# Kernel optimization log

Hardware: AMD Instinct MI355X
Metric: run time of the kernel (lower is better)

Reference implementation:

```python
import jax, jax.numpy as jnp
import numpy as np

N_HEAD = 8
T_THRESHOLD = 0.001


def setup_inputs() -> dict:
    key = jax.random.key(0)
    ks = jax.random.split(key, 5)
    B, N, NL, R = 4, 1024, 4, 256
    C = NL * R
    x = jax.random.normal(ks[0], (B, N, NL, R), dtype=jnp.float32)
    Wc = jax.random.normal(ks[1], (R, 3 * R), dtype=jnp.float32) * (1.0 / np.sqrt(R))
    bc = jnp.zeros((3 * R,), dtype=jnp.float32)
    Wp = jax.random.normal(ks[2], (C, C), dtype=jnp.float32) * (1.0 / np.sqrt(C))
    bp = jnp.zeros((C,), dtype=jnp.float32)
    return {"x": x, "Wc": Wc, "bc": bc, "Wp": Wp, "bp": bp}


def reference(x, Wc, bc, Wp, bp):
    B, N, NL, R = x.shape
    H = N_HEAD
    D = R // H  # head dim
    # shared per-level qkv projection: (B, N, NL, 3R)
    qkv = x @ Wc + bc
    q, k, v = jnp.split(qkv, 3, axis=-1)
    # split heads: (B, N, NL, H, D)
    q = q.reshape(B, N, NL, H, D)
    k = k.reshape(B, N, NL, H, D)
    v = v.reshape(B, N, NL, H, D)
    scale = 1.0 / np.sqrt(D).astype(np.float32)
    # per-level attention scores: (B, NL, H, N, N)
    att = jnp.einsum('bnlhd,bmlhd->blhnm', q, k) * scale
    att = jax.nn.softmax(att, axis=-1)
    # custom post-softmax thresholding (ReLU(softmax - T)); dropout is identity at eval
    att = jax.nn.relu(att - T_THRESHOLD)
    # multiply attentions across levels: low parent attention dooms the child
    comb = jnp.prod(att, axis=1)  # (B, H, N, N)
    # apply combined attention to each level's values: (B, N, NL, H, D)
    y = jnp.einsum('bhnm,bmlhd->bnlhd', comb, v)
    y = y.reshape(B, N, NL * H * D)  # (B, N, C)
    y = y @ Wp + bp  # c_proj; resid dropout identity at eval
    return y.reshape(B, N, NL, R)
```

## Files before the change

kernel.cpp:

```cpp
#include <hip/hip_runtime.h>

#define TTHR 0.001f
#define QSC2 0.25503486f
#define CAP 16
#define YSCALE 8388608.0f
#define YINV   1.1920928955078125e-07f

#if __has_builtin(__builtin_amdgcn_exp2f)
#define EXP2(x) __builtin_amdgcn_exp2f(x)
#else
#define EXP2(x) __expf((x) * 0.6931471805599453f)
#endif

typedef _Float16 half4v __attribute__((ext_vector_type(4)));
typedef _Float16 half8v __attribute__((ext_vector_type(8)));
typedef float f32x4 __attribute__((ext_vector_type(4)));

__device__ __forceinline__ int xcd_bid() {
  return (blockIdx.x & 7) * ((int)gridDim.x >> 3) + ((int)blockIdx.x >> 3);
}

__device__ __forceinline__ void stage_tile_s(const _Float16* __restrict__ gsrc,
                                             int rowstride, _Float16* lds, int tid)
{
  const int lane = tid & 63;
  const int w4 = (tid >> 6) << 2;
#pragma unroll
  for (int r = 0; r < 4; ++r) {
    const int p = (w4 + r) * 64 + lane;
    const int row = p >> 3, xg = p & 7;
    __builtin_amdgcn_global_load_lds(
        (const __attribute__((address_space(1))) void*)(gsrc + row * rowstride + ((xg ^ (row & 7)) << 3)),
        (__attribute__((address_space(3))) void*)(lds + (w4 + r) * 512),
        16, 0, 0);
  }
}

__device__ __forceinline__ void stage_tile64(const _Float16* __restrict__ gsrc,
                                             int rowstride, _Float16* lds, int tid)
{
  const int lane = tid & 63;
  const int w2 = (tid >> 6) << 1;
#pragma unroll
  for (int r = 0; r < 2; ++r) {
    const int p = (w2 + r) * 64 + lane;
    const int row = p >> 3, xg = p & 7;
    __builtin_amdgcn_global_load_lds(
        (const __attribute__((address_space(1))) void*)(gsrc + row * rowstride + ((xg ^ (row & 7)) << 3)),
        (__attribute__((address_space(3))) void*)(lds + (w2 + r) * 512),
        16, 0, 0);
  }
}

__device__ __forceinline__ void stage_q64_512(const _Float16* __restrict__ gsrc,
                                              _Float16* lds, int tid)
{
  const int lane = tid & 63, w = tid >> 6;
  const int p = (w << 6) + lane;
  const int row = p >> 3, xg = p & 7;
  __builtin_amdgcn_global_load_lds(
      (const __attribute__((address_space(1))) void*)(gsrc + row * 64 + ((xg ^ (row & 7)) << 3)),
      (__attribute__((address_space(3))) void*)(lds + (w << 9)),
      16, 0, 0);
}

__device__ __forceinline__ void stage_k128_512(const _Float16* __restrict__ gsrc,
                                               _Float16* lds, int tid)
{
  const int lane = tid & 63, w = tid >> 6;
#pragma unroll
  for (int r = 0; r < 2; ++r) {
    const int p = ((w << 1) + r) * 64 + lane;
    const int row = p >> 3, xg = p & 7;
    __builtin_amdgcn_global_load_lds(
        (const __attribute__((address_space(1))) void*)(gsrc + row * 64 + ((xg ^ (row & 7)) << 3)),
        (__attribute__((address_space(3))) void*)(lds + ((w << 1) + r) * 512),
        16, 0, 0);
  }
}

__global__ __launch_bounds__(256) void k_split_rm(
    const float* __restrict__ in, _Float16* __restrict__ oh,
    _Float16* __restrict__ ol, int n4)
{
  const int i = blockIdx.x * 256 + threadIdx.x;
  if (i >= n4) return;
  float4 v = ((const float4*)in)[i];
  half4v h = {(_Float16)v.x, (_Float16)v.y, (_Float16)v.z, (_Float16)v.w};
  half4v l = {(_Float16)(v.x - (float)h[0]), (_Float16)(v.y - (float)h[1]),
              (_Float16)(v.z - (float)h[2]), (_Float16)(v.w - (float)h[3])};
  ((half4v*)oh)[i] = h;
  ((half4v*)ol)[i] = l;
}

__global__ __launch_bounds__(256) void k_split_tr(
    const float* __restrict__ in, _Float16* __restrict__ oh,
    _Float16* __restrict__ ol, int K, int N)
{
  __shared__ float t[32][33];
  const int nb = N >> 5;
  const int n0 = (blockIdx.x % nb) << 5, k0 = (blockIdx.x / nb) << 5;
  const int r = threadIdx.x >> 3, c4 = (threadIdx.x & 7) << 2;
  float4 v = *(const float4*)&in[(k0 + r) * N + n0 + c4];
  t[r][c4] = v.x; t[r][c4 + 1] = v.y; t[r][c4 + 2] = v.z; t[r][c4 + 3] = v.w;
  __syncthreads();
  float a0 = t[c4][r], a1 = t[c4 + 1][r], a2 = t[c4 + 2][r], a3 = t[c4 + 3][r];
  half4v h = {(_Float16)a0, (_Float16)a1, (_Float16)a2, (_Float16)a3};
  half4v l = {(_Float16)(a0 - (float)h[0]), (_Float16)(a1 - (float)h[1]),
              (_Float16)(a2 - (float)h[2]), (_Float16)(a3 - (float)h[3])};
  *(half4v*)&oh[(n0 + r) * K + k0 + c4] = h;
  *(half4v*)&ol[(n0 + r) * K + k0 + c4] = l;
}

template<int EPI>
__global__ __launch_bounds__(256) void k_gemm_split(
    const _Float16* __restrict__ Ah, const _Float16* __restrict__ Al,
    const _Float16* __restrict__ Bh, const _Float16* __restrict__ Bl,
    const float* __restrict__ bias, int K, int kclog, int nbn,
    float* __restrict__ out, _Float16* __restrict__ Qs,
    _Float16* __restrict__ Ks, float* __restrict__ Vp)
{
  __shared__ __align__(16) _Float16 Asm[3][8192];
  __shared__ __align__(16) _Float16 Bsm[3][4096];
  const int tid = threadIdx.x, lane = tid & 63, w = tid >> 6;
  const int wr = w >> 1, wc = w & 1;
  const int lrow = lane & 15, lk = lane >> 4;
  const int bid = xcd_bid();
  const int mt = bid / nbn, ct = bid % nbn;
  const int m0 = mt << 7, c0 = ct << 6;

  const int nch = 3 << kclog;
  const int kcm = (1 << kclog) - 1;

  auto abase = [&](int c2) -> const _Float16* {
    const int phase = c2 >> kclog, kc = c2 & kcm;
    const _Float16* A = (phase == 2) ? Al : Ah;
    return A + (size_t)m0 * K + (kc << 6);
  };
  auto bbase = [&](int c2) -> const _Float16* {
    const int phase = c2 >> kclog, kc = c2 & kcm;
    const _Float16* B = (phase == 1) ? Bl : Bh;
    return B + (size_t)c0 * K + (kc << 6);
  };

  stage_tile_s(abase(0), K, Asm[0], tid);
  stage_tile64(bbase(0), K, Bsm[0], tid);
  stage_tile_s(abase(1), K, Asm[1], tid);
  stage_tile64(bbase(1), K, Bsm[1], tid);

  f32x4 acc[4][2] = {};
  int cur = 0;
#pragma unroll 1
  for (int ch = 0; ch < nch; ++ch) {
    if (ch + 1 < nch) { asm volatile("s_waitcnt vmcnt(6)" ::: "memory"); }
    else              { asm volatile("s_waitcnt vmcnt(0)" ::: "memory"); }
    __builtin_amdgcn_s_barrier();
    __builtin_amdgcn_sched_barrier(0);
#pragma unroll
    for (int ks = 0; ks < 2; ++ks) {
      half8v af[4], bf[2];
#pragma unroll
      for (int mi = 0; mi < 4; ++mi) {
        const int row = (wr << 6) + (mi << 4) + lrow;
        const int xg = ((ks << 2) + lk) ^ (row & 7);
        af[mi] = *(const half8v*)&Asm[cur][((row << 3) + xg) << 3];
      }
#pragma unroll
      for (int ni = 0; ni < 2; ++ni) {
        const int col = (wc << 5) + (ni << 4) + lrow;
        const int xg = ((ks << 2) + lk) ^ (col & 7);
        bf[ni] = *(const half8v*)&Bsm[cur][((col << 3) + xg) << 3];
      }
#pragma unroll
      for (int mi = 0; mi < 4; ++mi)
#pragma unroll
        for (int ni = 0; ni < 2; ++ni)
          acc[mi][ni] = __builtin_amdgcn_mfma_f32_16x16x32_f16(af[mi], bf[ni], acc[mi][ni], 0, 0, 0);
    }
    if (ch + 2 < nch) {
      int nb = cur + 2; if (nb >= 3) nb -= 3;
      stage_tile_s(abase(ch + 2), K, Asm[nb], tid);
      stage_tile64(bbase(ch + 2), K, Bsm[nb], tid);
    }
    ++cur; if (cur == 3) cur = 0;
  }

#pragma unroll
  for (int ni = 0; ni < 2; ++ni) {
    const int c = c0 + (wc << 5) + (ni << 4) + lrow;
    const float bv = bias[c];
    if (EPI == 0) {
#pragma unroll
      for (int mi = 0; mi < 4; ++mi)
#pragma unroll
        for (int reg = 0; reg < 4; ++reg) {
          const int m = m0 + (wr << 6) + (mi << 4) + (lk << 2) + reg;
          out[m * 1024 + c] = acc[mi][ni][reg] * YINV + bv;
        }
    } else {
      const int part = c >> 8, cc = c & 255;
      const int h = cc >> 5, d = cc & 31;
#pragma unroll
      for (int mi = 0; mi < 4; ++mi)
#pragma unroll
        for (int reg = 0; reg < 4; ++reg) {
          const int m = m0 + (wr << 6) + (mi << 4) + (lk << 2) + reg;
          const int b = m >> 12, n = (m >> 2) & 1023, l = m & 3;
          const int panel = b * 32 + l * 8 + h;
          float v = acc[mi][ni][reg] + bv;
          if (part == 2) {
            Vp[(panel << 15) + n * 32 + d] = v;
          } else {
            _Float16* dst = part ? Ks : Qs;
            if (!part) v *= QSC2;
            _Float16 hv = (_Float16)v;
            _Float16 lv = (_Float16)(v - (float)hv);
            dst[(panel << 16) + n * 64 + d] = hv;
            dst[(panel << 16) + n * 64 + 32 + d] = lv;
          }
        }
    }
  }
}

__global__ __launch_bounds__(512) void k_att(
    const _Float16* __restrict__ Qs, const _Float16* __restrict__ Ks,
    int* __restrict__ ccnt, unsigned short* __restrict__ cidx,
    float* __restrict__ cval)
{
  __shared__ __align__(16) _Float16 Qres[4][4096];
  __shared__ __align__(16) _Float16 Kb[2][8192];
  __shared__ float Zsh[4][64];
  __shared__ float tzs[4][64];
  __shared__ float rz[64];
  __shared__ int lcnt[64];
  const int tid = threadIdx.x, lane = tid & 63, w = tid >> 6;
  const int wr = w >> 2, wc = w & 3;
  const int lrow = lane & 15, lk = lane >> 4;
  const int s = (blockIdx.x & 7) * 64 + ((int)blockIdx.x >> 3);
  const int bh = s >> 4, rt = s & 15;
  const int b = bh >> 3, h = bh & 7;
  const int pbase = b * 32 + h;

#pragma unroll
  for (int l = 0; l < 4; ++l)
    stage_q64_512(Qs + ((pbase + l * 8) << 16) + (rt << 12), Qres[l], tid);
  stage_k128_512(Ks + (pbase << 16), Kb[0], tid);
  if (tid < 256) Zsh[tid >> 6][tid & 63] = 0.0f;
  __syncthreads();

  const int kstA[3] = {0, 0, 4}, kstB[3] = {0, 4, 0};
  float rsum[2][4] = {};
  float prod[2][2][4];

#pragma unroll 1
  for (int it = 0; it < 64; ++it) {
    const int cur = it & 1;
    const int pass = it >> 5;
    const int l  = pass ? ((it - 32) & 3) : (it >> 3);
    const int ct = pass ? ((it - 32) >> 2) : (it & 7);
    if (it < 63) {
      const int t2 = it + 1;
      const int l2  = (t2 < 32) ? (t2 >> 3) : ((t2 - 32) & 3);
      const int ct2 = (t2 < 32) ? (t2 & 7) : ((t2 - 32) >> 2);
      stage_k128_512(Ks + ((pbase + l2 * 8) << 16) + (ct2 << 13), Kb[cur ^ 1], tid);
    }
    if (pass && l == 0 && tid < 64) lcnt[tid] = 0;

    f32x4 acc[2][2] = {};
#pragma unroll
    for (int ks = 0; ks < 3; ++ks) {
      half8v af[2], bf[2];
#pragma unroll
      for (int mi = 0; mi < 2; ++mi) {
        const int row = (wr << 5) + (mi << 4) + lrow;
        const int xg = (kstA[ks] + lk) ^ (row & 7);
        af[mi] = *(const half8v*)&Qres[l][((row << 3) + xg) << 3];
      }
#pragma unroll
      for (int ni = 0; ni < 2; ++ni) {
        const int col = (wc << 5) + (ni << 4) + lrow;
        const int xg = (kstB[ks] + lk) ^ (col & 7);
        bf[ni] = *(const half8v*)&Kb[cur][((col << 3) + xg) << 3];
      }
#pragma unroll
      for (int mi = 0; mi < 2; ++mi)
#pragma unroll
        for (int ni = 0; ni < 2; ++ni)
          acc[mi][ni] = __builtin_amdgcn_mfma_f32_16x16x32_f16(af[mi], bf[ni], acc[mi][ni], 0, 0, 0);
    }

    if (!pass) {
#pragma unroll
      for (int mi = 0; mi < 2; ++mi)
#pragma unroll
        for (int reg = 0; reg < 4; ++reg)
#pragma unroll
          for (int ni = 0; ni < 2; ++ni)
            rsum[mi][reg] += EXP2(acc[mi][ni][reg]);
      if ((it & 7) == 7) {
#pragma unroll
        for (int mi = 0; mi < 2; ++mi)
#pragma unroll
          for (int reg = 0; reg < 4; ++reg) {
            float v = rsum[mi][reg];
            v += __shfl_xor(v, 1, 64);
            v += __shfl_xor(v, 2, 64);
            v += __shfl_xor(v, 4, 64);
            v += __shfl_xor(v, 8, 64);
            if (lrow == 0)
              atomicAdd(&Zsh[l][(wr << 5) + (mi << 4) + (lk << 2) + reg], v);
            rsum[mi][reg] = 0.0f;
          }
      }
    } else {
#pragma unroll
      for (int mi = 0; mi < 2; ++mi)
#pragma unroll
        for (int reg = 0; reg < 4; ++reg) {
          const float tzv = tzs[l][(wr << 5) + (mi << 4) + (lk << 2) + reg];
#pragma unroll
          for (int ni = 0; ni < 2; ++ni) {
            const float e = fmaxf(EXP2(acc[mi][ni][reg]) - tzv, 0.0f);
            prod[mi][ni][reg] = (l == 0) ? e : prod[mi][ni][reg] * e;
          }
        }
      if (l == 3) {
#pragma unroll
        for (int mi = 0; mi < 2; ++mi)
#pragma unroll
          for (int ni = 0; ni < 2; ++ni)
#pragma unroll
            for (int reg = 0; reg < 4; ++reg) {
              const int rloc = (wr << 5) + (mi << 4) + (lk << 2) + reg;
              const float v = prod[mi][ni][reg] * rz[rloc];
              if (v > 0.0f) {
                const int slot = atomicAdd(&lcnt[rloc], 1);
                if (slot < CAP) {
                  const int rowc = (bh << 10) + (rt << 6) + rloc;
                  const int mglob = (ct << 7) + (wc << 5) + (ni << 4) + lrow;
                  cidx[(rowc * 8 + ct) * CAP + slot] = (unsigned short)mglob;
                  cval[(rowc * 8 + ct) * CAP + slot] = v * YSCALE;
                }
              }
            }
        __syncthreads();
        if (tid < 64)
          ccnt[((bh << 10) + (rt << 6) + tid) * 8 + ct] = min(lcnt[tid], CAP);
      }
    }
    __syncthreads();
    if (it == 31) {
      if (tid < 256) tzs[tid >> 6][tid & 63] = TTHR * Zsh[tid >> 6][tid & 63];
      if (tid < 64)
        rz[tid] = 1.0f / ((Zsh[0][tid] * Zsh[1][tid]) * (Zsh[2][tid] * Zsh[3][tid]));
      __syncthreads();
    }
  }
}

__global__ __launch_bounds__(512) void k_pv(
    const float* __restrict__ Vp, const int* __restrict__ ccnt,
    const unsigned short* __restrict__ cidx, const float* __restrict__ cval,
    _Float16* __restrict__ ysh, _Float16* __restrict__ ysl)
{
  const int rowc = blockIdx.x * 8 + (threadIdx.x >> 6);
  const int lane = threadIdx.x & 63;
  const int bh = rowc >> 10, n = rowc & 1023;
  const int b = bh >> 3, h = bh & 7;
  const int l0 = lane >> 5, d = lane & 31;
  const float* vA = Vp + ((b * 32 + l0 * 8 + h) << 15) + d;
  const float* vB = vA + (16 << 15);
  float y0 = 0.f, y1 = 0.f;
  for (int mcj = 0; mcj < 8; ++mcj) {
    const int cnt = ccnt[rowc * 8 + mcj];
    const int off = (rowc * 8 + mcj) * CAP;
    for (int i = 0; i < cnt; ++i) {
      const int m = cidx[off + i];
      const float wv = cval[off + i];
      y0 = fmaf(wv, vA[m * 32], y0);
      y1 = fmaf(wv, vB[m * 32], y1);
    }
  }
  const int idx = ((b << 10) + n) * 1024 + l0 * 256 + h * 32 + d;
  _Float16 h0 = (_Float16)y0;
  ysh[idx] = h0;
  ysl[idx] = (_Float16)(y0 - (float)h0);
  _Float16 h1 = (_Float16)y1;
  ysh[idx + 512] = h1;
  ysl[idx + 512] = (_Float16)(y1 - (float)h1);
}

extern "C" void kernel_launch(void* const* d_in, const int* in_sizes, int n_in,
                              void* d_out, int out_size, void* d_ws, size_t ws_size,
                              hipStream_t stream)
{
  const float* x  = (const float*)d_in[0];
  const float* Wc = (const float*)d_in[1];
  const float* bc = (const float*)d_in[2];
  const float* Wp = (const float*)d_in[3];
  const float* bp = (const float*)d_in[4];
  float* out = (float*)d_out;
  (void)in_sizes; (void)n_in; (void)out_size;

  if (ws_size < 98828288ull) return;
  char* wsb = (char*)d_ws;
  float*          Vp   = (float*)wsb;
  _Float16*       Qs   = (_Float16*)(wsb + 16777216);
  _Float16*       Ks   = (_Float16*)(wsb + 33554432);
  _Float16*       xh   = (_Float16*)(wsb + 50855936);
  _Float16*       xl   = (_Float16*)(wsb + 59244544);
  int*            ccnt = (int*)(wsb + 67633152);
  unsigned short* cidx = (unsigned short*)(wsb + 68681728);
  float*          cval = (float*)(wsb + 77070336);
  _Float16*       Wch  = (_Float16*)(wsb + 93847552);
  _Float16*       Wcl  = (_Float16*)(wsb + 94240768);
  _Float16*       Wph  = (_Float16*)(wsb + 94633984);
  _Float16*       Wpl  = (_Float16*)(wsb + 96731136);

  k_split_rm<<<dim3(4096), dim3(256), 0, stream>>>(x, xh, xl, 1048576);
  k_split_tr<<<dim3(192), dim3(256), 0, stream>>>(Wc, Wch, Wcl, 256, 768);
  k_split_tr<<<dim3(1024), dim3(256), 0, stream>>>(Wp, Wph, Wpl, 1024, 1024);
  k_gemm_split<1><<<dim3(1536), dim3(256), 0, stream>>>(
      xh, xl, Wch, Wcl, bc, 256, 2, 12, nullptr, Qs, Ks, Vp);
  k_att<<<dim3(512), dim3(512), 0, stream>>>(Qs, Ks, ccnt, cidx, cval);
  k_pv<<<dim3(4096), dim3(512), 0, stream>>>(Vp, ccnt, cidx, cval, xh, xl);
  k_gemm_split<0><<<dim3(512), dim3(256), 0, stream>>>(
      xh, xl, Wph, Wpl, bp, 1024, 4, 16, out, nullptr, nullptr, nullptr);
}
```

Before: 228.5 us.

## Load Q/K fragments directly from global in attention kernel, drop LDS staging

The attention kernel stops staging Q and K tiles into LDS via async global-to-LDS copies and instead reads MFMA fragments straight from global memory into registers. It also skips the Q-low correction term in the first pass, where only row sums are needed, and replaces the per-tile LDS counter plus barrier with global atomics on a count buffer that is zeroed by a memset before launch. This removes most per-iteration block barriers and the LDS footprint, and launch bounds are raised so more blocks can be resident. In exchange it relies on L1/L2 for the repeated K reads, adds a memset, and uses global atomics, so compaction slot order becomes nondeterministic.

Measured after the change: 356.8 us. 1.56x slower.

```diff
diff --git a/kernel.cpp b/kernel.cpp
--- a/kernel.cpp
+++ b/kernel.cpp
@@ -48,33 +48,6 @@
     __builtin_amdgcn_global_load_lds(
         (const __attribute__((address_space(1))) void*)(gsrc + row * rowstride + ((xg ^ (row & 7)) << 3)),
         (__attribute__((address_space(3))) void*)(lds + (w2 + r) * 512),
-        16, 0, 0);
-  }
-}
-
-__device__ __forceinline__ void stage_q64_512(const _Float16* __restrict__ gsrc,
-                                              _Float16* lds, int tid)
-{
-  const int lane = tid & 63, w = tid >> 6;
-  const int p = (w << 6) + lane;
-  const int row = p >> 3, xg = p & 7;
-  __builtin_amdgcn_global_load_lds(
-      (const __attribute__((address_space(1))) void*)(gsrc + row * 64 + ((xg ^ (row & 7)) << 3)),
-      (__attribute__((address_space(3))) void*)(lds + (w << 9)),
-      16, 0, 0);
-}
-
-__device__ __forceinline__ void stage_k128_512(const _Float16* __restrict__ gsrc,
-                                               _Float16* lds, int tid)
-{
-  const int lane = tid & 63, w = tid >> 6;
-#pragma unroll
-  for (int r = 0; r < 2; ++r) {
-    const int p = ((w << 1) + r) * 64 + lane;
-    const int row = p >> 3, xg = p & 7;
-    __builtin_amdgcn_global_load_lds(
-        (const __attribute__((address_space(1))) void*)(gsrc + row * 64 + ((xg ^ (row & 7)) << 3)),
-        (__attribute__((address_space(3))) void*)(lds + ((w << 1) + r) * 512),
         16, 0, 0);
   }
 }
@@ -223,17 +196,14 @@
   }
 }
 
-__global__ __launch_bounds__(512) void k_att(
+__global__ __launch_bounds__(512, 4) void k_att(
     const _Float16* __restrict__ Qs, const _Float16* __restrict__ Ks,
     int* __restrict__ ccnt, unsigned short* __restrict__ cidx,
     float* __restrict__ cval)
 {
-  __shared__ __align__(16) _Float16 Qres[4][4096];
-  __shared__ __align__(16) _Float16 Kb[2][8192];
   __shared__ float Zsh[4][64];
   __shared__ float tzs[4][64];
   __shared__ float rz[64];
-  __shared__ int lcnt[64];
   const int tid = threadIdx.x, lane = tid & 63, w = tid >> 6;
   const int wr = w >> 2, wc = w & 3;
   const int lrow = lane & 15, lk = lane >> 4;
@@ -242,52 +212,55 @@
   const int b = bh >> 3, h = bh & 7;
   const int pbase = b * 32 + h;
 
-#pragma unroll
-  for (int l = 0; l < 4; ++l)
-    stage_q64_512(Qs + ((pbase + l * 8) << 16) + (rt << 12), Qres[l], tid);
-  stage_k128_512(Ks + (pbase << 16), Kb[0], tid);
+  const _Float16* Qp0 = Qs + ((size_t)pbase << 16) + (rt << 12);
+  const _Float16* Kp0 = Ks + ((size_t)pbase << 16);
+  int qoff[2], koff[2];
+#pragma unroll
+  for (int mi = 0; mi < 2; ++mi)
+    qoff[mi] = ((wr << 5) + (mi << 4) + lrow) * 64 + lk * 8;
+#pragma unroll
+  for (int ni = 0; ni < 2; ++ni)
+    koff[ni] = ((wc << 5) + (ni << 4) + lrow) * 64 + lk * 8;
+
   if (tid < 256) Zsh[tid >> 6][tid & 63] = 0.0f;
   __syncthreads();
 
-  const int kstA[3] = {0, 0, 4}, kstB[3] = {0, 4, 0};
   float rsum[2][4] = {};
   float prod[2][2][4];
 
 #pragma unroll 1
   for (int it = 0; it < 64; ++it) {
-    const int cur = it & 1;
     const int pass = it >> 5;
     const int l  = pass ? ((it - 32) & 3) : (it >> 3);
     const int ct = pass ? ((it - 32) >> 2) : (it & 7);
-    if (it < 63) {
-      const int t2 = it + 1;
-      const int l2  = (t2 < 32) ? (t2 >> 3) : ((t2 - 32) & 3);
-      const int ct2 = (t2 < 32) ? (t2 & 7) : ((t2 - 32) >> 2);
-      stage_k128_512(Ks + ((pbase + l2 * 8) << 16) + (ct2 << 13), Kb[cur ^ 1], tid);
-    }
-    if (pass && l == 0 && tid < 64) lcnt[tid] = 0;
-
+    const _Float16* qb = Qp0 + ((size_t)l << 19);
+    const _Float16* kb = Kp0 + ((size_t)l << 19) + (ct << 13);
+
+    half8v qh[2], kh[2], kl[2];
+#pragma unroll
+    for (int mi = 0; mi < 2; ++mi) qh[mi] = *(const half8v*)(qb + qoff[mi]);
+#pragma unroll
+    for (int ni = 0; ni < 2; ++ni) {
+      kh[ni] = *(const half8v*)(kb + koff[ni]);
+      kl[ni] = *(const half8v*)(kb + koff[ni] + 32);
+    }
     f32x4 acc[2][2] = {};
 #pragma unroll
-    for (int ks = 0; ks < 3; ++ks) {
-      half8v af[2], bf[2];
-#pragma unroll
-      for (int mi = 0; mi < 2; ++mi) {
-        const int row = (wr << 5) + (mi << 4) + lrow;
-        const int xg = (kstA[ks] + lk) ^ (row & 7);
-        af[mi] = *(const half8v*)&Qres[l][((row << 3) + xg) << 3];
-      }
+    for (int mi = 0; mi < 2; ++mi)
 #pragma unroll
       for (int ni = 0; ni < 2; ++ni) {
-        const int col = (wc << 5) + (ni << 4) + lrow;
-        const int xg = (kstB[ks] + lk) ^ (col & 7);
-        bf[ni] = *(const half8v*)&Kb[cur][((col << 3) + xg) << 3];
-      }
+        acc[mi][ni] = __builtin_amdgcn_mfma_f32_16x16x32_f16(qh[mi], kh[ni], acc[mi][ni], 0, 0, 0);
+        acc[mi][ni] = __builtin_amdgcn_mfma_f32_16x16x32_f16(qh[mi], kl[ni], acc[mi][ni], 0, 0, 0);
+      }
+    if (pass) {
+      half8v ql[2];
+#pragma unroll
+      for (int mi = 0; mi < 2; ++mi) ql[mi] = *(const half8v*)(qb + qoff[mi] + 32);
 #pragma unroll
       for (int mi = 0; mi < 2; ++mi)
 #pragma unroll
         for (int ni = 0; ni < 2; ++ni)
-          acc[mi][ni] = __builtin_amdgcn_mfma_f32_16x16x32_f16(af[mi], bf[ni], acc[mi][ni], 0, 0, 0);
+          acc[mi][ni] = __builtin_amdgcn_mfma_f32_16x16x32_f16(ql[mi], kh[ni], acc[mi][ni], 0, 0, 0);
     }
 
     if (!pass) {
@@ -295,9 +268,7 @@
       for (int mi = 0; mi < 2; ++mi)
 #pragma unroll
         for (int reg = 0; reg < 4; ++reg)
-#pragma unroll
-          for (int ni = 0; ni < 2; ++ni)
-            rsum[mi][reg] += EXP2(acc[mi][ni][reg]);
+          rsum[mi][reg] += EXP2(acc[mi][0][reg]) + EXP2(acc[mi][1][reg]);
       if ((it & 7) == 7) {
 #pragma unroll
         for (int mi = 0; mi < 2; ++mi)
@@ -313,48 +284,49 @@
             rsum[mi][reg] = 0.0f;
           }
       }
+      if (it == 31) {
+        __syncthreads();
+        if (tid < 256) tzs[tid >> 6][tid & 63] = TTHR * Zsh[tid >> 6][tid & 63];
+        if (tid < 64)
+          rz[tid] = 1.0f / ((Zsh[0][tid] * Zsh[1][tid]) * (Zsh[2][tid] * Zsh[3][tid]));
+        __syncthreads();
+      }
     } else {
 #pragma unroll
-      for (int mi = 0; mi < 2; ++mi)
-#pragma unroll
-        for (int reg = 0; reg < 4; ++reg) {
-          const float tzv = tzs[l][(wr << 5) + (mi << 4) + (lk << 2) + reg];
+      for (int mi = 0; mi < 2; ++mi) {
+        const float4 tzv = *(const float4*)&tzs[l][(wr << 5) + (mi << 4) + (lk << 2)];
+        const float tza[4] = {tzv.x, tzv.y, tzv.z, tzv.w};
+#pragma unroll
+        for (int reg = 0; reg < 4; ++reg)
 #pragma unroll
           for (int ni = 0; ni < 2; ++ni) {
-            const float e = fmaxf(EXP2(acc[mi][ni][reg]) - tzv, 0.0f);
+            const float e = fmaxf(EXP2(acc[mi][ni][reg]) - tza[reg], 0.0f);
             prod[mi][ni][reg] = (l == 0) ? e : prod[mi][ni][reg] * e;
           }
-        }
+      }
       if (l == 3) {
 #pragma unroll
-        for (int mi = 0; mi < 2; ++mi)
+        for (int mi = 0; mi < 2; ++mi) {
+          const float4 rzv = *(const float4*)&rz[(wr << 5) + (mi << 4) + (lk << 2)];
+          const float rza[4] = {rzv.x, rzv.y, rzv.z, rzv.w};
 #pragma unroll
           for (int ni = 0; ni < 2; ++ni)
 #pragma unroll
             for (int reg = 0; reg < 4; ++reg) {
-              const int rloc = (wr << 5) + (mi << 4) + (lk << 2) + reg;
-              const float v = prod[mi][ni][reg] * rz[rloc];
+              const float v = prod[mi][ni][reg] * rza[reg];
               if (v > 0.0f) {
-                const int slot = atomicAdd(&lcnt[rloc], 1);
+                const int rloc = (wr << 5) + (mi << 4) + (lk << 2) + reg;
+                const int rowc = (bh << 10) + (rt << 6) + rloc;
+                const int slot = atomicAdd(&ccnt[rowc * 8 + ct], 1);
                 if (slot < CAP) {
-                  const int rowc = (bh << 10) + (rt << 6) + rloc;
                   const int mglob = (ct << 7) + (wc << 5) + (ni << 4) + lrow;
                   cidx[(rowc * 8 + ct) * CAP + slot] = (unsigned short)mglob;
                   cval[(rowc * 8 + ct) * CAP + slot] = v * YSCALE;
                 }
               }
             }
-        __syncthreads();
-        if (tid < 64)
-          ccnt[((bh << 10) + (rt << 6) + tid) * 8 + ct] = min(lcnt[tid], CAP);
-      }
-    }
-    __syncthreads();
-    if (it == 31) {
-      if (tid < 256) tzs[tid >> 6][tid & 63] = TTHR * Zsh[tid >> 6][tid & 63];
-      if (tid < 64)
-        rz[tid] = 1.0f / ((Zsh[0][tid] * Zsh[1][tid]) * (Zsh[2][tid] * Zsh[3][tid]));
-      __syncthreads();
+        }
+      }
     }
   }
 }
@@ -373,7 +345,7 @@
   const float* vB = vA + (16 << 15);
   float y0 = 0.f, y1 = 0.f;
   for (int mcj = 0; mcj < 8; ++mcj) {
-    const int cnt = ccnt[rowc * 8 + mcj];
+    const int cnt = min(ccnt[rowc * 8 + mcj], CAP);
     const int off = (rowc * 8 + mcj) * CAP;
     for (int i = 0; i < cnt; ++i) {
       const int m = cidx[off + i];
@@ -418,6 +390,7 @@
   _Float16*       Wph  = (_Float16*)(wsb + 94633984);
   _Float16*       Wpl  = (_Float16*)(wsb + 96731136);
 
+  hipMemsetAsync(ccnt, 0, 1048576, stream);
   k_split_rm<<<dim3(4096), dim3(256), 0, stream>>>(x, xh, xl, 1048576);
   k_split_tr<<<dim3(192), dim3(256), 0, stream>>>(Wc, Wch, Wcl, 256, 768);
   k_split_tr<<<dim3(1024), dim3(256), 0, stream>>>(Wp, Wph, Wpl, 1024, 1024);
```
